# Kernel optimization log

Measured on AMD Instinct MI355X. Metric: run time of the kernel, lower is better.

## Reference

```python
import jax, jax.numpy as jnp
import numpy as np

DIM = 1024
NUM_HEADS = 16
HEAD_DIM = DIM // NUM_HEADS
SCALING = HEAD_DIM ** (-0.5)


def setup_inputs() -> dict:
    key = jax.random.key(0)
    ks = jax.random.split(key, 9)
    B, S = 2, 2048
    s = DIM ** -0.5  # ~ torch Linear init scale
    inp = {
        "x": jax.random.normal(ks[0], (B, S, DIM), dtype=jnp.float32),
        "wq": jax.random.uniform(ks[1], (DIM, DIM), jnp.float32, -s, s),
        "bq": jax.random.uniform(ks[2], (DIM,), jnp.float32, -s, s),
        "wk": jax.random.uniform(ks[3], (DIM, DIM), jnp.float32, -s, s),
        "bk": jax.random.uniform(ks[4], (DIM,), jnp.float32, -s, s),
        "wv": jax.random.uniform(ks[5], (DIM, DIM), jnp.float32, -s, s),
        "bv": jax.random.uniform(ks[6], (DIM,), jnp.float32, -s, s),
        "wo": jax.random.uniform(ks[7], (DIM, DIM), jnp.float32, -s, s),
        "bo": jax.random.uniform(ks[8], (DIM,), jnp.float32, -s, s),
    }
    return inp


def reference(x, wq, bq, wk, bk, wv, bv, wo, bo):
    B, S, D = x.shape
    # projections (weights stored [out,in] like torch Linear -> x @ W.T + b)
    q = (x @ wq.T + bq).reshape(B, S, NUM_HEADS, HEAD_DIM)
    k = (x @ wk.T + bk).reshape(B, S, NUM_HEADS, HEAD_DIM)
    v = (x @ wv.T + bv).reshape(B, S, NUM_HEADS, HEAD_DIM)
    # [B,H,S,S] scores, scaled
    scores = jnp.einsum("bqhd,bkhd->bhqk", q, k) * SCALING
    attn = jax.nn.softmax(scores, axis=-1)
    # dropout p=0.0 (eval): identity
    out = jnp.einsum("bhqk,bkhd->bqhd", attn, v).reshape(B, S, D)
    return out @ wo.T + bo
```

## Files before the change

### kernel.cpp

```cpp
#include <hip/hip_runtime.h>

#define DIM 1024
#define NHEADS 16
#define HDIM 64
#define BATCH 2
#define SEQ 2048
#define MTOT (BATCH*SEQ)
#define QSCALE 0.18033688011112042f
#define XN ((size_t)MTOT*DIM)
#define WN ((size_t)DIM*DIM)

typedef __attribute__((ext_vector_type(8))) short short8;
typedef __attribute__((ext_vector_type(4))) float f32x4;
typedef __attribute__((ext_vector_type(16))) float f32x16;
typedef __attribute__((ext_vector_type(2))) int int2v;

static __device__ __forceinline__ unsigned short bf16rne(float f) {
    unsigned u = __builtin_bit_cast(unsigned, f);
    return (unsigned short)((u + 0x7fffu + ((u >> 16) & 1u)) >> 16);
}

static __device__ __forceinline__ void gld16(const void* g, void* l) {
    __builtin_amdgcn_global_load_lds((const __attribute__((address_space(1))) void*)g,
                                     (__attribute__((address_space(3))) void*)l, 16, 0, 0);
}

__global__ __launch_bounds__(256)
void prep(const float* __restrict__ x, const float* __restrict__ wq, const float* __restrict__ wk,
          const float* __restrict__ wv, const float* __restrict__ wo, unsigned short* __restrict__ dst)
{
    const size_t i = ((size_t)blockIdx.x*256 + threadIdx.x)*8;
    const float* s; size_t o;
    if (i < XN)           { s = x;  o = i; }
    else if (i < XN+WN)   { s = wq; o = i - XN; }
    else if (i < XN+2*WN) { s = wk; o = i - XN - WN; }
    else if (i < XN+3*WN) { s = wv; o = i - XN - 2*WN; }
    else                  { s = wo; o = i - XN - 3*WN; }
    float4 a = *(const float4*)(s + o);
    float4 b = *(const float4*)(s + o + 4);
    uint4 w;
    w.x = (unsigned)bf16rne(a.x) | ((unsigned)bf16rne(a.y) << 16);
    w.y = (unsigned)bf16rne(a.z) | ((unsigned)bf16rne(a.w) << 16);
    w.z = (unsigned)bf16rne(b.x) | ((unsigned)bf16rne(b.y) << 16);
    w.w = (unsigned)bf16rne(b.z) | ((unsigned)bf16rne(b.w) << 16);
    *(uint4*)&dst[i] = w;
}

template<int FUSED>
__global__ __launch_bounds__(256)
void gemm_qkv(const unsigned short* __restrict__ A,
              const unsigned short* __restrict__ W0, const unsigned short* __restrict__ W1,
              const unsigned short* __restrict__ W2,
              const float* __restrict__ b0, const float* __restrict__ b1, const float* __restrict__ b2,
              unsigned short* __restrict__ o0, unsigned short* __restrict__ o1, unsigned short* __restrict__ o2,
              float* __restrict__ fo)
{
    __shared__ __align__(16) unsigned short As[2][4096];
    __shared__ __align__(16) unsigned short Bs[2][4096];
    const int t = threadIdx.x, wid = t >> 6, lane = t & 63;
    const int lr = lane & 15, lg = lane >> 4;
    const int m0 = blockIdx.y * 128;
    int n0, widx;
    const unsigned short* W; const float* bias; float scale;
    if constexpr (FUSED) {
        widx = blockIdx.x >> 3; n0 = (blockIdx.x & 7) * 128;
        W    = widx == 0 ? W0 : (widx == 1 ? W1 : W2);
        bias = widx == 0 ? b0 : (widx == 1 ? b1 : b2);
        scale = widx == 0 ? QSCALE : 1.0f;
    } else {
        widx = 0; n0 = blockIdx.x * 128; W = W0; bias = b0; scale = 1.0f;
    }
    const int wm = wid >> 1, wn = wid & 1;
    const int f0 = 2*wid, f1 = f0 + 1;
    const unsigned short* Ag0 = A + (size_t)(m0 + f0*16 + lr)*DIM + lg*8;
    const unsigned short* Ag1 = A + (size_t)(m0 + f1*16 + lr)*DIM + lg*8;
    const unsigned short* Bg0 = W + (size_t)(n0 + f0*16 + lr)*DIM + lg*8;
    const unsigned short* Bg1 = W + (size_t)(n0 + f1*16 + lr)*DIM + lg*8;

    f32x4 acc[4][4] = {};

    gld16(Ag0, &As[0][f0*512]); gld16(Ag1, &As[0][f1*512]);
    gld16(Bg0, &Bs[0][f0*512]); gld16(Bg1, &Bs[0][f1*512]);

    for (int it = 0; it < DIM/32; ++it) {
        __syncthreads();
        if (it + 1 < DIM/32) {
            const int nbf = (it+1)&1; const int ko = (it+1)*32;
            gld16(Ag0 + ko, &As[nbf][f0*512]); gld16(Ag1 + ko, &As[nbf][f1*512]);
            gld16(Bg0 + ko, &Bs[nbf][f0*512]); gld16(Bg1 + ko, &Bs[nbf][f1*512]);
        }
        const int cb = it & 1;
        short8 af[4], bf[4];
        #pragma unroll
        for (int i = 0; i < 4; ++i) af[i] = *(const short8*)&As[cb][(wm*4+i)*512 + lane*8];
        #pragma unroll
        for (int i = 0; i < 4; ++i) bf[i] = *(const short8*)&Bs[cb][(wn*4+i)*512 + lane*8];
        #pragma unroll
        for (int mb = 0; mb < 4; ++mb)
            #pragma unroll
            for (int nb = 0; nb < 4; ++nb)
                acc[mb][nb] = __builtin_amdgcn_mfma_f32_16x16x32_bf16(af[mb], bf[nb], acc[mb][nb], 0, 0, 0);
    }

    #pragma unroll
    for (int nb = 0; nb < 4; ++nb) {
        const int col = n0 + wn*64 + nb*16 + lr;
        const float bv = bias[col];
        #pragma unroll
        for (int mb = 0; mb < 4; ++mb) {
            #pragma unroll
            for (int j = 0; j < 4; ++j) {
                const int row = m0 + wm*64 + mb*16 + lg*4 + j;
                float v = (acc[mb][nb][j] + bv) * scale;
                if constexpr (FUSED) {
                    unsigned short* out = widx == 0 ? o0 : (widx == 1 ? o1 : o2);
                    out[(size_t)row*DIM + col] = bf16rne(v);
                } else {
                    fo[(size_t)row*DIM + col] = v;
                }
            }
        }
    }
}

__global__ __launch_bounds__(256)
void transpose_v(const unsigned short* __restrict__ V, unsigned short* __restrict__ Vt)
{
    __shared__ unsigned short tile[64][66];
    const int t  = threadIdx.x;
    const int st = blockIdx.x;
    const int bh = blockIdx.y;
    const int b = bh >> 4, h = bh & 15;
    const int sr = t >> 3;
    const int dc = (t & 7) * 8;

    #pragma unroll
    for (int r = 0; r < 2; ++r) {
        const int s = r*32 + sr;
        short8 v = *(const short8*)(V + (size_t)(b*SEQ + st*64 + s)*DIM + h*HDIM + dc);
        #pragma unroll
        for (int e = 0; e < 8; ++e) tile[s][dc + e] = (unsigned short)v[e];
    }
    __syncthreads();
    #pragma unroll
    for (int r = 0; r < 2; ++r) {
        const int d = r*32 + sr;
        short8 ov;
        #pragma unroll
        for (int e = 0; e < 8; ++e) ov[e] = (short)tile[dc + e][d];
        *(short8*)(Vt + (size_t)bh*HDIM*SEQ + (size_t)d*SEQ + st*64 + dc) = ov;
    }
}

__global__ __launch_bounds__(256)
void attn_mfma2(const unsigned short* __restrict__ Q, const unsigned short* __restrict__ Kg,
                const unsigned short* __restrict__ Vt, unsigned short* __restrict__ O)
{
    __shared__ __align__(16) unsigned short Ks[2][4096];
    __shared__ __align__(16) unsigned short Vs[2][4096];
    const int t = threadIdx.x, wid = t >> 6, lane = t & 63;
    const int l31 = lane & 31, h = lane >> 5;
    const int qt = blockIdx.x, bh = blockIdx.y, b = bh >> 4, hh = bh & 15;
    const size_t qkbase = (size_t)b*SEQ*DIM + (size_t)hh*HDIM;
    const unsigned short* Qb = Q + qkbase;
    const unsigned short* Kb = Kg + qkbase;
    const unsigned short* Vb = Vt + (size_t)bh*HDIM*SEQ;
    unsigned short*       Ob = O + qkbase;
    const int q0 = qt*128 + wid*32;

    short8 qf[4];
    #pragma unroll
    for (int ds = 0; ds < 4; ++ds)
        qf[ds] = *(const short8*)&Qb[(size_t)(q0 + l31)*DIM + ds*16 + h*8];

    const int f0 = 2*wid, f1 = f0 + 1;
    const unsigned short* Kg0 = &Kb[(size_t)((f0>>2)*32 + l31)*DIM + (f0&3)*16 + h*8];
    const unsigned short* Kg1 = &Kb[(size_t)((f1>>2)*32 + l31)*DIM + (f1&3)*16 + h*8];
    const unsigned short* Vg0 = &Vb[(size_t)((f0>>2)*32 + l31)*SEQ + (f0&3)*16 + h*8];
    const unsigned short* Vg1 = &Vb[(size_t)((f1>>2)*32 + l31)*SEQ + (f1&3)*16 + h*8];

    f32x16 ctx0 = {}, ctx1 = {};
    float lsum = 0.0f;

    gld16(Kg0, &Ks[0][f0*512]); gld16(Kg1, &Ks[0][f1*512]);
    gld16(Vg0, &Vs[0][f0*512]); gld16(Vg1, &Vs[0][f1*512]);

    for (int kt = 0; kt < SEQ/64; ++kt) {
        __syncthreads();
        if (kt + 1 < SEQ/64) {
            const int nbf = (kt+1)&1;
            const size_t ko = (size_t)(kt+1)*64;
            gld16(Kg0 + ko*DIM, &Ks[nbf][f0*512]); gld16(Kg1 + ko*DIM, &Ks[nbf][f1*512]);
            gld16(Vg0 + ko,     &Vs[nbf][f0*512]); gld16(Vg1 + ko,     &Vs[nbf][f1*512]);
        }
        const int cb = kt & 1;

        f32x16 s0 = {}, s1 = {};
        __builtin_amdgcn_s_setprio(1);
        #pragma unroll
        for (int ds = 0; ds < 4; ++ds) {
            short8 kf0 = *(const short8*)&Ks[cb][ds*512 + lane*8];
            short8 kf1 = *(const short8*)&Ks[cb][(4+ds)*512 + lane*8];
            s0 = __builtin_amdgcn_mfma_f32_32x32x16_bf16(kf0, qf[ds], s0, 0, 0, 0);
            s1 = __builtin_amdgcn_mfma_f32_32x32x16_bf16(kf1, qf[ds], s1, 0, 0, 0);
        }
        __builtin_amdgcn_s_setprio(0);

        float rsum = 0.0f;
        unsigned pw[2][4][2];
        #pragma unroll
        for (int r1 = 0; r1 < 4; ++r1)
            #pragma unroll
            for (int tt = 0; tt < 2; ++tt) {
                float pa_ = __builtin_amdgcn_exp2f(s0[4*r1+2*tt]);
                float pb_ = __builtin_amdgcn_exp2f(s0[4*r1+2*tt+1]);
                float pc_ = __builtin_amdgcn_exp2f(s1[4*r1+2*tt]);
                float pd_ = __builtin_amdgcn_exp2f(s1[4*r1+2*tt+1]);
                rsum += (pa_ + pb_) + (pc_ + pd_);
                unsigned w0, w1;
                asm("v_cvt_pk_bf16_f32 %0, %1, %2" : "=v"(w0) : "v"(pa_), "v"(pb_));
                asm("v_cvt_pk_bf16_f32 %0, %1, %2" : "=v"(w1) : "v"(pc_), "v"(pd_));
                pw[0][r1][tt] = w0;
                pw[1][r1][tt] = w1;
            }
        rsum += __shfl_xor(rsum, 32);
        lsum += rsum;

        short8 pa4[4];
        #pragma unroll
        for (int ss = 0; ss < 4; ++ss) {
            union { short8 s8; unsigned u[4]; } pu;
            #pragma unroll
            for (int tt = 0; tt < 2; ++tt) {
                int2v sw = __builtin_amdgcn_permlane32_swap(
                    (int)pw[ss>>1][2*(ss&1)][tt], (int)pw[ss>>1][2*(ss&1)+1][tt], false, false);
                pu.u[tt]     = (unsigned)sw[0];
                pu.u[2 + tt] = (unsigned)sw[1];
            }
            pa4[ss] = pu.s8;
        }

        __builtin_amdgcn_s_setprio(1);
        #pragma unroll
        for (int ss = 0; ss < 4; ++ss) {
            short8 vf0 = *(const short8*)&Vs[cb][ss*512 + lane*8];
            short8 vf1 = *(const short8*)&Vs[cb][(4+ss)*512 + lane*8];
            ctx0 = __builtin_amdgcn_mfma_f32_32x32x16_bf16(pa4[ss], vf0, ctx0, 0, 0, 0);
            ctx1 = __builtin_amdgcn_mfma_f32_32x32x16_bf16(pa4[ss], vf1, ctx1, 0, 0, 0);
        }
        __builtin_amdgcn_s_setprio(0);
    }

    const float linv = 1.0f / lsum;
    #pragma unroll
    for (int r = 0; r < 16; ++r) {
        const int qrow = (r&3) + 8*(r>>2) + 4*h;
        const float nm = __shfl(linv, qrow);
        unsigned short* p = &Ob[(size_t)(q0 + qrow)*DIM + l31];
        p[0]  = bf16rne(ctx0[r] * nm);
        p[32] = bf16rne(ctx1[r] * nm);
    }
}

extern "C" void kernel_launch(void* const* d_in, const int* in_sizes, int n_in,
                              void* d_out, int out_size, void* d_ws, size_t ws_size,
                              hipStream_t stream) {
    const float* x  = (const float*)d_in[0];
    const float* wq = (const float*)d_in[1];
    const float* bq = (const float*)d_in[2];
    const float* wk = (const float*)d_in[3];
    const float* bk = (const float*)d_in[4];
    const float* wv = (const float*)d_in[5];
    const float* bv = (const float*)d_in[6];
    const float* wo = (const float*)d_in[7];
    const float* bo = (const float*)d_in[8];
    float* out = (float*)d_out;

    unsigned short* Xb  = (unsigned short*)d_ws;
    unsigned short* Wqb = Xb  + XN;
    unsigned short* Wkb = Wqb + WN;
    unsigned short* Wvb = Wkb + WN;
    unsigned short* Wob = Wvb + WN;
    unsigned short* Qb  = Wob + WN;
    unsigned short* Kb  = Qb  + XN;
    unsigned short* Vb  = Kb  + XN;
    unsigned short* Vtb = Vb  + XN;
    unsigned short* Cb  = Vb;

    prep<<<4096, 256, 0, stream>>>(x, wq, wk, wv, wo, Xb);

    gemm_qkv<1><<<dim3(24, 32), 256, 0, stream>>>(Xb, Wqb, Wkb, Wvb, bq, bk, bv,
                                                  Qb, Kb, Vb, nullptr);

    transpose_v<<<dim3(SEQ/64, BATCH*NHEADS), 256, 0, stream>>>(Vb, Vtb);
    attn_mfma2<<<dim3(SEQ/128, BATCH*NHEADS), 256, 0, stream>>>(Qb, Kb, Vtb, Cb);

    gemm_qkv<0><<<dim3(8, 32), 256, 0, stream>>>(Cb, Wob, nullptr, nullptr, bo, nullptr, nullptr,
                                                 nullptr, nullptr, nullptr, out);
}
```

Baseline: 158.9 us.

## Swizzle block order across XCDs, add 64-row output GEMM, remove prefetch branches

Remaps block indices in the QKV GEMM, attention and output GEMM so that consecutively dispatched blocks (round-robined across XCDs) share operand tiles, aiming for better L2 reuse. Adds a dedicated output-projection kernel with 64x128 tiles, doubling the grid to 512 blocks to fill more CUs than the previous 256-block launch. Replaces the conditional prefetch with an unconditional wrapped load (last iteration reloads tile 0) to drop a branch, and raises wave priority around the MFMA blocks. The wrapped prefetch adds one redundant load per block, and the smaller output tiles reduce arithmetic reuse per block.

```diff
diff --git a/kernel.cpp b/kernel.cpp
--- a/kernel.cpp
+++ b/kernel.cpp
@@ -46,30 +46,28 @@
     *(uint4*)&dst[i] = w;
 }
 
-template<int FUSED>
 __global__ __launch_bounds__(256)
 void gemm_qkv(const unsigned short* __restrict__ A,
               const unsigned short* __restrict__ W0, const unsigned short* __restrict__ W1,
               const unsigned short* __restrict__ W2,
               const float* __restrict__ b0, const float* __restrict__ b1, const float* __restrict__ b2,
-              unsigned short* __restrict__ o0, unsigned short* __restrict__ o1, unsigned short* __restrict__ o2,
-              float* __restrict__ fo)
+              unsigned short* __restrict__ o0, unsigned short* __restrict__ o1, unsigned short* __restrict__ o2)
 {
     __shared__ __align__(16) unsigned short As[2][4096];
     __shared__ __align__(16) unsigned short Bs[2][4096];
     const int t = threadIdx.x, wid = t >> 6, lane = t & 63;
     const int lr = lane & 15, lg = lane >> 4;
-    const int m0 = blockIdx.y * 128;
-    int n0, widx;
-    const unsigned short* W; const float* bias; float scale;
-    if constexpr (FUSED) {
-        widx = blockIdx.x >> 3; n0 = (blockIdx.x & 7) * 128;
-        W    = widx == 0 ? W0 : (widx == 1 ? W1 : W2);
-        bias = widx == 0 ? b0 : (widx == 1 ? b1 : b2);
-        scale = widx == 0 ? QSCALE : 1.0f;
-    } else {
-        widx = 0; n0 = blockIdx.x * 128; W = W0; bias = b0; scale = 1.0f;
-    }
+    const int bid = blockIdx.y * 24 + blockIdx.x;
+    const int swz = (bid & 7) * 96 + (bid >> 3);
+    const int sx = swz % 24, sy = swz / 24;
+    const int widx = sx >> 3;
+    const int n0 = (sx & 7) << 7;
+    const int m0 = sy << 7;
+    const unsigned short* W = widx == 0 ? W0 : (widx == 1 ? W1 : W2);
+    const float* bias        = widx == 0 ? b0 : (widx == 1 ? b1 : b2);
+    const float scale        = widx == 0 ? QSCALE : 1.0f;
+    unsigned short* out      = widx == 0 ? o0 : (widx == 1 ? o1 : o2);
+
     const int wm = wid >> 1, wn = wid & 1;
     const int f0 = 2*wid, f1 = f0 + 1;
     const unsigned short* Ag0 = A + (size_t)(m0 + f0*16 + lr)*DIM + lg*8;
@@ -84,8 +82,8 @@
 
     for (int it = 0; it < DIM/32; ++it) {
         __syncthreads();
-        if (it + 1 < DIM/32) {
-            const int nbf = (it+1)&1; const int ko = (it+1)*32;
+        {
+            const int nbf = (it+1)&1; const int ko = ((it+1)&31)*32;
             gld16(Ag0 + ko, &As[nbf][f0*512]); gld16(Ag1 + ko, &As[nbf][f1*512]);
             gld16(Bg0 + ko, &Bs[nbf][f0*512]); gld16(Bg1 + ko, &Bs[nbf][f1*512]);
         }
@@ -95,11 +93,13 @@
         for (int i = 0; i < 4; ++i) af[i] = *(const short8*)&As[cb][(wm*4+i)*512 + lane*8];
         #pragma unroll
         for (int i = 0; i < 4; ++i) bf[i] = *(const short8*)&Bs[cb][(wn*4+i)*512 + lane*8];
+        __builtin_amdgcn_s_setprio(1);
         #pragma unroll
         for (int mb = 0; mb < 4; ++mb)
             #pragma unroll
             for (int nb = 0; nb < 4; ++nb)
                 acc[mb][nb] = __builtin_amdgcn_mfma_f32_16x16x32_bf16(af[mb], bf[nb], acc[mb][nb], 0, 0, 0);
+        __builtin_amdgcn_s_setprio(0);
     }
 
     #pragma unroll
@@ -111,13 +111,69 @@
             #pragma unroll
             for (int j = 0; j < 4; ++j) {
                 const int row = m0 + wm*64 + mb*16 + lg*4 + j;
-                float v = (acc[mb][nb][j] + bv) * scale;
-                if constexpr (FUSED) {
-                    unsigned short* out = widx == 0 ? o0 : (widx == 1 ? o1 : o2);
-                    out[(size_t)row*DIM + col] = bf16rne(v);
-                } else {
-                    fo[(size_t)row*DIM + col] = v;
-                }
+                out[(size_t)row*DIM + col] = bf16rne((acc[mb][nb][j] + bv) * scale);
+            }
+        }
+    }
+}
+
+__global__ __launch_bounds__(256)
+void gemm_o(const unsigned short* __restrict__ A, const unsigned short* __restrict__ W,
+            const float* __restrict__ bias, float* __restrict__ fo)
+{
+    __shared__ __align__(16) unsigned short As[2][2048];
+    __shared__ __align__(16) unsigned short Bs[2][4096];
+    const int t = threadIdx.x, wid = t >> 6, lane = t & 63;
+    const int lr = lane & 15, lg = lane >> 4;
+    const int bid = blockIdx.y * 8 + blockIdx.x;
+    const int swz = (bid & 7) * 64 + (bid >> 3);
+    const int n0 = (swz & 7) << 7;
+    const int m0 = (swz >> 3) << 6;
+    const int wm = wid >> 1, wn = wid & 1;
+
+    const int fa = wid;
+    const int g0 = 2*wid, g1 = g0 + 1;
+    const unsigned short* Ag  = A + (size_t)(m0 + fa*16 + lr)*DIM + lg*8;
+    const unsigned short* Bg0 = W + (size_t)(n0 + g0*16 + lr)*DIM + lg*8;
+    const unsigned short* Bg1 = W + (size_t)(n0 + g1*16 + lr)*DIM + lg*8;
+
+    f32x4 acc[2][4] = {};
+
+    gld16(Ag, &As[0][fa*512]);
+    gld16(Bg0, &Bs[0][g0*512]); gld16(Bg1, &Bs[0][g1*512]);
+
+    for (int it = 0; it < DIM/32; ++it) {
+        __syncthreads();
+        {
+            const int nbf = (it+1)&1; const int ko = ((it+1)&31)*32;
+            gld16(Ag + ko, &As[nbf][fa*512]);
+            gld16(Bg0 + ko, &Bs[nbf][g0*512]); gld16(Bg1 + ko, &Bs[nbf][g1*512]);
+        }
+        const int cb = it & 1;
+        short8 af[2], bf[4];
+        #pragma unroll
+        for (int i = 0; i < 2; ++i) af[i] = *(const short8*)&As[cb][(wm*2+i)*512 + lane*8];
+        #pragma unroll
+        for (int i = 0; i < 4; ++i) bf[i] = *(const short8*)&Bs[cb][(wn*4+i)*512 + lane*8];
+        __builtin_amdgcn_s_setprio(1);
+        #pragma unroll
+        for (int mb = 0; mb < 2; ++mb)
+            #pragma unroll
+            for (int nb = 0; nb < 4; ++nb)
+                acc[mb][nb] = __builtin_amdgcn_mfma_f32_16x16x32_bf16(af[mb], bf[nb], acc[mb][nb], 0, 0, 0);
+        __builtin_amdgcn_s_setprio(0);
+    }
+
+    #pragma unroll
+    for (int nb = 0; nb < 4; ++nb) {
+        const int col = n0 + wn*64 + nb*16 + lr;
+        const float bv = bias[col];
+        #pragma unroll
+        for (int mb = 0; mb < 2; ++mb) {
+            #pragma unroll
+            for (int j = 0; j < 4; ++j) {
+                const int row = m0 + wm*32 + mb*16 + lg*4 + j;
+                fo[(size_t)row*DIM + col] = acc[mb][nb][j] + bv;
             }
         }
     }
@@ -160,7 +216,10 @@
     __shared__ __align__(16) unsigned short Vs[2][4096];
     const int t = threadIdx.x, wid = t >> 6, lane = t & 63;
     const int l31 = lane & 31, h = lane >> 5;
-    const int qt = blockIdx.x, bh = blockIdx.y, b = bh >> 4, hh = bh & 15;
+    const int bid = blockIdx.y * 16 + blockIdx.x;
+    const int swz = (bid & 7) * 64 + (bid >> 3);
+    const int qt = swz & 15, bh = swz >> 4;
+    const int b = bh >> 4, hh = bh & 15;
     const size_t qkbase = (size_t)b*SEQ*DIM + (size_t)hh*HDIM;
     const unsigned short* Qb = Q + qkbase;
     const unsigned short* Kb = Kg + qkbase;
@@ -187,11 +246,13 @@
 
     for (int kt = 0; kt < SEQ/64; ++kt) {
         __syncthreads();
-        if (kt + 1 < SEQ/64) {
+        {
             const int nbf = (kt+1)&1;
-            const size_t ko = (size_t)(kt+1)*64;
-            gld16(Kg0 + ko*DIM, &Ks[nbf][f0*512]); gld16(Kg1 + ko*DIM, &Ks[nbf][f1*512]);
-            gld16(Vg0 + ko,     &Vs[nbf][f0*512]); gld16(Vg1 + ko,     &Vs[nbf][f1*512]);
+            const int ktn = (kt+1) & (SEQ/64 - 1);
+            const size_t koK = (size_t)ktn * 64 * DIM;
+            const size_t koV = (size_t)ktn * 64;
+            gld16(Kg0 + koK, &Ks[nbf][f0*512]); gld16(Kg1 + koK, &Ks[nbf][f1*512]);
+            gld16(Vg0 + koV, &Vs[nbf][f0*512]); gld16(Vg1 + koV, &Vs[nbf][f1*512]);
         }
         const int cb = kt & 1;
 
@@ -289,12 +350,10 @@
 
     prep<<<4096, 256, 0, stream>>>(x, wq, wk, wv, wo, Xb);
 
-    gemm_qkv<1><<<dim3(24, 32), 256, 0, stream>>>(Xb, Wqb, Wkb, Wvb, bq, bk, bv,
-                                                  Qb, Kb, Vb, nullptr);
+    gemm_qkv<<<dim3(24, 32), 256, 0, stream>>>(Xb, Wqb, Wkb, Wvb, bq, bk, bv, Qb, Kb, Vb);
 
     transpose_v<<<dim3(SEQ/64, BATCH*NHEADS), 256, 0, stream>>>(Vb, Vtb);
     attn_mfma2<<<dim3(SEQ/128, BATCH*NHEADS), 256, 0, stream>>>(Qb, Kb, Vtb, Cb);
 
-    gemm_qkv<0><<<dim3(8, 32), 256, 0, stream>>>(Cb, Wob, nullptr, nullptr, bo, nullptr, nullptr,
-                                                 nullptr, nullptr, nullptr, out);
-}
+    gemm_o<<<dim3(8, 64), 256, 0, stream>>>(Cb, Wob, bo, out);
+}
```

Result: faster. 151.5 us (-4.6%).
